# Kernel tuning notes

Measured on AMD Instinct MI355X. Metric: run time of the kernel, lower is better.

The kernel has to match this reference:

```python
import jax, jax.numpy as jnp
import numpy as np

IN_FEATURES = 4096
OUT_FEATURES = 8192
GROUP_SIZE = 16
NUM_GROUPS = IN_FEATURES * OUT_FEATURES // GROUP_SIZE  # 2_097_152


def block_dequantize_2bit(packed, normalization):
    # packed: [G, group_size//4] int32 holding uint8 values; norm: [G, 1] fp16
    shifts = jnp.arange(4, dtype=packed.dtype) * 2  # bit offsets 0,2,4,6
    # unpacked column 4k+i comes from packed column k, bits 2i..2i+1
    u = ((packed[:, :, None] >> shifts) & 3).astype(jnp.float32)  # [G, gs/4, 4]
    u = u.reshape(packed.shape[0], -1)  # [G, group_size]
    norm = normalization.astype(jnp.float32)
    return (u / 3.0) * (2.0 * norm) - norm  # [G, group_size]


def setup_inputs() -> dict:
    key = jax.random.key(0)
    k_x, k_q, k_n, k_b = jax.random.split(key, 4)
    x = jax.random.normal(k_x, (256, IN_FEATURES), dtype=jnp.float32)
    # packed 2-bit weights: random bytes (store as int32 for clean bit ops in jax)
    weight_q2 = jax.random.randint(k_q, (NUM_GROUPS, GROUP_SIZE // 4), 0, 256, dtype=jnp.int32)
    # per-group normalization (abs-max), positive, fp16 as in the module buffer
    weight_norm = (jax.random.uniform(k_n, (NUM_GROUPS, 1), dtype=jnp.float32) * 0.05 + 1e-4).astype(jnp.float16)
    bias = jax.random.normal(k_b, (OUT_FEATURES,), dtype=jnp.float32) * 0.01
    return {"x": x, "weight_q2": weight_q2, "weight_norm": weight_norm, "bias": bias}


def reference(x, weight_q2, weight_norm, bias):
    weight = block_dequantize_2bit(weight_q2, weight_norm).reshape(OUT_FEATURES, IN_FEATURES)
    return jnp.dot(x.astype(jnp.float32), weight.T) + bias
```

## Files before the change

### kernel.cpp

```cpp
#include <hip/hip_runtime.h>
#include <hip/hip_bf16.h>
#include <hip/hip_fp16.h>

#define IN_F   4096
#define OUT_F  8192
#define M_ROWS 256
#define SLAB   128
#define NSLAB  16

typedef __attribute__((ext_vector_type(8))) short  short8;
typedef __attribute__((ext_vector_type(4))) float  float4v;

union BF8 { uint4 u; short8 s; };

typedef __attribute__((address_space(1))) const unsigned int glb_uint;
typedef __attribute__((address_space(3))) unsigned int       lds_uint;

__device__ inline void gld_lds16(const void* g, void* l) {
    __builtin_amdgcn_global_load_lds((glb_uint*)g, (lds_uint*)l, 16, 0, 0);
}

__device__ inline unsigned int pack_bf16(float lo, float hi) {
    return __builtin_amdgcn_perm(__float_as_uint(hi), __float_as_uint(lo), 0x07060302u);
}

__global__ void cvt_x_kernel(const float* __restrict__ x, unsigned short* __restrict__ xb) {
    int i = blockIdx.x * blockDim.x + threadIdx.x;
    if (i < (M_ROWS * IN_F) / 4) {
        float4 v = ((const float4*)x)[i];
        uint2 o;
        o.x = pack_bf16(v.x, v.y);
        o.y = pack_bf16(v.z, v.w);
        ((uint2*)xb)[i] = o;
    }
}

template <bool XB>
__global__ __launch_bounds__(512, 4) void gemm2bit_kernel(
    const float*           __restrict__ xf,
    const unsigned short*  __restrict__ xb,
    const int*             __restrict__ wq,
    const void*            __restrict__ wnorm,
    const float*           __restrict__ bias,
    float*                 __restrict__ out)
{
    __shared__ unsigned short ldsA[2][2][64 * SLAB];

    const int t    = threadIdx.x;
    const int n0   = blockIdx.x * 64;
    const int m0   = blockIdx.y * 64;
    const int wave = t >> 6;
    const int lane = t & 63;
    const int gw   = wave & 3;
    const int grp  = wave >> 2;
    const int l15  = lane & 15;
    const int quad = lane >> 4;

    const float cand0 = *(const float*)wnorm;
    const bool  nf32  = (cand0 > 1e-5f && cand0 < 0.1f);
    const float*  nF = (const float*)wnorm;
    const __half* nH = (const __half*)wnorm;

    const int   ncol = n0 + gw * 16 + l15;
    const float bv   = bias[ncol];
    const int   kgrp = grp * (IN_F / 2);

    const int* wqW  = wq + ncol * (IN_F / 4) + (kgrp >> 2) + quad * 2;
    const int  nrmW = ncol * (IN_F / 16) + (kgrp >> 4) + (quad >> 1);

    const int srow4 = lane >> 4;
    const int sj    = lane & 15;

    int stv[4];
#pragma unroll
    for (int ks = 0; ks < 4; ++ks) {
        const int c = ks * 4 + quad;
        stv[ks] = ((c & 8) | ((c ^ (l15 & 7)) & 7)) * 8;
    }
    int fb[4];
#pragma unroll
    for (int i = 0; i < 4; ++i) fb[i] = (i * 16 + l15) * SLAB;

    float4v acc[4] = {};

    auto stage = [&](int s, int b) {
        const int kbase = kgrp + s * SLAB;
        if constexpr (XB) {
#pragma unroll
            for (int c = 0; c < 4; ++c) {
                const int R  = gw * 16 + c * 4 + srow4;
                const int lc = (sj & 8) | ((sj ^ (R & 7)) & 7);
                const unsigned short* g = xb + (m0 + R) * IN_F + kbase + lc * 8;
                gld_lds16(g, &ldsA[grp][b][(gw * 16 + c * 4) * SLAB]);
            }
        } else {
#pragma unroll
            for (int c = 0; c < 4; ++c) {
                const int R  = gw * 16 + c * 4 + srow4;
                const int lc = (sj & 8) | ((sj ^ (R & 7)) & 7);
                const float4* g = (const float4*)(xf + (m0 + R) * IN_F + kbase + lc * 8);
                float4 v0 = g[0], v1 = g[1];
                uint4 o;
                o.x = pack_bf16(v0.x, v0.y); o.y = pack_bf16(v0.z, v0.w);
                o.z = pack_bf16(v1.x, v1.y); o.w = pack_bf16(v1.z, v1.w);
                *(uint4*)&ldsA[grp][b][R * SLAB + sj * 8] = o;
            }
        }
    };

    auto load_b = [&](int s, int2 (&q)[4], float (&n)[4]) {
#pragma unroll
        for (int ks = 0; ks < 4; ++ks) {
            q[ks] = *(const int2*)(wqW + s * 32 + ks * 8);
            const int gi = nrmW + s * 8 + ks * 2;
            n[ks] = nf32 ? nF[gi] : __half2float(nH[gi]);
        }
    };

    stage(0, 0);
    int2  qn[4];
    float nn[4];
    load_b(0, qn, nn);

    for (int s = 0; s < NSLAB; ++s) {
        __syncthreads();

        if (s + 1 < NSLAB) stage(s + 1, (s + 1) & 1);

        int2  qc[4];
        float nc[4];
#pragma unroll
        for (int ks = 0; ks < 4; ++ks) { qc[ks] = qn[ks]; nc[ks] = nn[ks]; }
        const int sl = (s + 1 < NSLAB) ? (s + 1) : s;
        load_b(sl, qn, nn);

        const unsigned short* A = ldsA[grp][s & 1];
#pragma unroll
        for (int ks = 0; ks < 4; ++ks) {
            const float nnv = nc[ks];
            const float sc  = nnv * (2.0f / 3.0f);
            const int qx = qc[ks].x, qy = qc[ks].y;

            float f0 = fmaf((float)((qx      ) & 3), sc, -nnv);
            float f1 = fmaf((float)((qx >>  2) & 3), sc, -nnv);
            float f2 = fmaf((float)((qx >>  4) & 3), sc, -nnv);
            float f3 = fmaf((float)((qx >>  6) & 3), sc, -nnv);
            float f4 = fmaf((float)((qy      ) & 3), sc, -nnv);
            float f5 = fmaf((float)((qy >>  2) & 3), sc, -nnv);
            float f6 = fmaf((float)((qy >>  4) & 3), sc, -nnv);
            float f7 = fmaf((float)((qy >>  6) & 3), sc, -nnv);

            BF8 bb;
            bb.u.x = pack_bf16(f0, f1);
            bb.u.y = pack_bf16(f2, f3);
            bb.u.z = pack_bf16(f4, f5);
            bb.u.w = pack_bf16(f6, f7);

#pragma unroll
            for (int i = 0; i < 4; ++i) {
                short8 a = *(const short8*)&A[fb[i] + stv[ks]];
                acc[i] = __builtin_amdgcn_mfma_f32_16x16x32_bf16(a, bb.s, acc[i], 0, 0, 0);
            }
        }
    }

    __syncthreads();
    float* red = (float*)&ldsA[0][0][0];
    if (grp == 1) {
#pragma unroll
        for (int i = 0; i < 4; ++i)
            *(float4*)&red[(gw * 64 + lane) * 16 + i * 4] = *(float4*)&acc[i];
    }
    __syncthreads();
    if (grp == 0) {
#pragma unroll
        for (int i = 0; i < 4; ++i) {
            const float4 o = *(const float4*)&red[(gw * 64 + lane) * 16 + i * 4];
            const int row0 = m0 + i * 16 + quad * 4;
            out[(row0 + 0) * OUT_F + ncol] = acc[i][0] + o.x + bv;
            out[(row0 + 1) * OUT_F + ncol] = acc[i][1] + o.y + bv;
            out[(row0 + 2) * OUT_F + ncol] = acc[i][2] + o.z + bv;
            out[(row0 + 3) * OUT_F + ncol] = acc[i][3] + o.w + bv;
        }
    }
}

extern "C" void kernel_launch(void* const* d_in, const int* in_sizes, int n_in,
                              void* d_out, int out_size, void* d_ws, size_t ws_size,
                              hipStream_t stream) {
    const float* x    = (const float*)d_in[0];
    const int*   wq   = (const int*)d_in[1];
    const void*  wn   = (const void*)d_in[2];
    const float* bias = (const float*)d_in[3];
    float*       out  = (float*)d_out;

    const bool use_ws = ws_size >= (size_t)(M_ROWS * IN_F * sizeof(unsigned short));

    dim3 grid(OUT_F / 64, M_ROWS / 64);

    if (use_ws) {
        unsigned short* xb = (unsigned short*)d_ws;
        cvt_x_kernel<<<dim3((M_ROWS * IN_F / 4 + 255) / 256), 256, 0, stream>>>(x, xb);
        gemm2bit_kernel<true><<<grid, 512, 0, stream>>>(nullptr, xb, wq, wn, bias, out);
    } else {
        gemm2bit_kernel<false><<<grid, 512, 0, stream>>>(x, nullptr, wq, wn, bias, out);
    }
}
```

Measured before the change: 152.9 us.

## Transpose packed weights and norms per call for coalesced 32x32 MFMA GEMM

Adds per-call kernels that transpose the packed 2-bit weights and the per-group norms into K-major layouts in workspace. A new GEMM kernel then reads them coalesced across output columns. It uses 32x32x16 bf16 MFMA and splits K four ways across waves, reducing partials through LDS. The transposes add extra full passes over the weight (about 32 MB read and 32 MB written) and a fp32 norm copy on every call, in exchange for better access patterns in the main kernel.

```diff
diff --git a/kernel.cpp b/kernel.cpp
--- a/kernel.cpp
+++ b/kernel.cpp
@@ -5,11 +5,10 @@
 #define IN_F   4096
 #define OUT_F  8192
 #define M_ROWS 256
-#define SLAB   128
-#define NSLAB  16
-
-typedef __attribute__((ext_vector_type(8))) short  short8;
-typedef __attribute__((ext_vector_type(4))) float  float4v;
+
+typedef __attribute__((ext_vector_type(8)))  short short8;
+typedef __attribute__((ext_vector_type(4)))  float float4v;
+typedef __attribute__((ext_vector_type(16))) float float16v;
 
 union BF8 { uint4 u; short8 s; };
 
@@ -23,6 +22,7 @@
 __device__ inline unsigned int pack_bf16(float lo, float hi) {
     return __builtin_amdgcn_perm(__float_as_uint(hi), __float_as_uint(lo), 0x07060302u);
 }
+
 
 __global__ void cvt_x_kernel(const float* __restrict__ x, unsigned short* __restrict__ xb) {
     int i = blockIdx.x * blockDim.x + threadIdx.x;
@@ -35,6 +35,196 @@
     }
 }
 
+__global__ __launch_bounds__(256) void transpose_wq_kernel(
+    const int* __restrict__ wq, int* __restrict__ wqT) {
+    __shared__ int tile[64][65];
+    const int t   = threadIdx.x;
+    const int kq0 = blockIdx.x * 64;
+    const int n0  = blockIdx.y * 64;
+    {
+        const int r  = t >> 4;
+        const int c4 = (t & 15) * 4;
+#pragma unroll
+        for (int it = 0; it < 4; ++it) {
+            const int rr = it * 16 + r;
+            const int4 v = *(const int4*)(wq + (n0 + rr) * (IN_F / 4) + kq0 + c4);
+            tile[rr][c4 + 0] = v.x; tile[rr][c4 + 1] = v.y;
+            tile[rr][c4 + 2] = v.z; tile[rr][c4 + 3] = v.w;
+        }
+    }
+    __syncthreads();
+    {
+        const int kr = t >> 6;
+        const int nc = t & 63;
+#pragma unroll
+        for (int it = 0; it < 16; ++it) {
+            const int kk = it * 4 + kr;
+            wqT[(kq0 + kk) * OUT_F + n0 + nc] = tile[nc][kk];
+        }
+    }
+}
+
+__global__ __launch_bounds__(256) void transpose_nrm_kernel(
+    const void* __restrict__ nrm, float* __restrict__ nT) {
+    __shared__ float tile[64][65];
+    const float cand0 = *(const float*)nrm;
+    const bool  nf32  = (cand0 > 1e-5f && cand0 < 0.1f);
+    const float*  nF = (const float*)nrm;
+    const __half* nH = (const __half*)nrm;
+    const int t   = threadIdx.x;
+    const int kg0 = blockIdx.x * 64;
+    const int n0  = blockIdx.y * 64;
+#pragma unroll
+    for (int it = 0; it < 16; ++it) {
+        const int idx = it * 256 + t;
+        const int r = idx >> 6, c = idx & 63;
+        const int gi = (n0 + r) * (IN_F / 16) + kg0 + c;
+        tile[r][c] = nf32 ? nF[gi] : __half2float(nH[gi]);
+    }
+    __syncthreads();
+#pragma unroll
+    for (int it = 0; it < 16; ++it) {
+        const int idx = it * 256 + t;
+        const int kr = idx >> 6, nc = idx & 63;
+        nT[(kg0 + kr) * OUT_F + n0 + nc] = tile[nc][kr];
+    }
+}
+
+__global__ __launch_bounds__(512, 4) void gemm2bit_t_kernel(
+    const unsigned short* __restrict__ xb,
+    const int*            __restrict__ wqT,
+    const float*          __restrict__ nT,
+    const float*          __restrict__ bias,
+    float*                __restrict__ out)
+{
+    __shared__ unsigned short smA[4][2][64 * 64];
+
+    const int t    = threadIdx.x;
+    const int wave = t >> 6;
+    const int lane = t & 63;
+    const int nw   = wave & 1;
+    const int kg   = wave >> 1;
+    const int n0   = blockIdx.x * 64;
+    const int m0   = blockIdx.y * 64;
+    const int l31  = lane & 31;
+    const int kh   = lane >> 5;
+
+    const int   ncol = n0 + nw * 32 + l31;
+    const float bv   = bias[ncol];
+    const int   kbase = kg * 1024;
+
+    const int*   qptr = wqT + ((kbase >> 2) + kh * 2) * OUT_F + ncol;
+    const float* nptr = nT  + (kbase >> 4) * OUT_F + ncol;
+
+    const int srow = nw * 32 + (lane >> 3);
+    const int schk = lane & 7;
+    const unsigned short* gA =
+        xb + (m0 + srow) * IN_F + kbase + ((schk ^ (srow & 7)) << 3);
+
+    const int fswz  = l31 & 7;
+    const int frow0 = l31 * 64;
+    const int frow1 = (32 + l31) * 64;
+
+    float16v acc0 = {}, acc1 = {};
+
+    auto stage = [&](int s, int b) {
+        unsigned short* dst = &smA[kg][b][(nw * 32) * 64];
+        const unsigned short* src = gA + s * 64;
+#pragma unroll
+        for (int c = 0; c < 4; ++c)
+            gld_lds16(src + c * 8 * IN_F, dst + c * 8 * 64);
+    };
+
+    int qA[4], qB[4]; float nv[4];
+    auto load_b = [&](int s) {
+#pragma unroll
+        for (int w = 0; w < 4; ++w) {
+            const int g16 = s * 4 + w;
+            qA[w] = qptr[(g16 * 4) * OUT_F];
+            qB[w] = qptr[(g16 * 4 + 1) * OUT_F];
+            nv[w] = nptr[g16 * OUT_F];
+        }
+    };
+
+    stage(0, 0);
+    load_b(0);
+
+    for (int s = 0; s < 16; ++s) {
+        __syncthreads();
+
+        if (s + 1 < 16) stage(s + 1, (s + 1) & 1);
+
+        int qAc[4], qBc[4]; float nvc[4];
+#pragma unroll
+        for (int w = 0; w < 4; ++w) { qAc[w] = qA[w]; qBc[w] = qB[w]; nvc[w] = nv[w]; }
+        load_b((s + 1 < 16) ? s + 1 : s);
+
+        const unsigned short* A = smA[kg][s & 1];
+#pragma unroll
+        for (int w = 0; w < 4; ++w) {
+            const float nn = nvc[w];
+            const float sc = nn * (2.0f / 3.0f);
+            const int qx = qAc[w], qy = qBc[w];
+
+            float f0 = fmaf((float)((qx      ) & 3), sc, -nn);
+            float f1 = fmaf((float)((qx >>  2) & 3), sc, -nn);
+            float f2 = fmaf((float)((qx >>  4) & 3), sc, -nn);
+            float f3 = fmaf((float)((qx >>  6) & 3), sc, -nn);
+            float f4 = fmaf((float)((qy      ) & 3), sc, -nn);
+            float f5 = fmaf((float)((qy >>  2) & 3), sc, -nn);
+            float f6 = fmaf((float)((qy >>  4) & 3), sc, -nn);
+            float f7 = fmaf((float)((qy >>  6) & 3), sc, -nn);
+
+            BF8 bb;
+            bb.u.x = pack_bf16(f0, f1);
+            bb.u.y = pack_bf16(f2, f3);
+            bb.u.z = pack_bf16(f4, f5);
+            bb.u.w = pack_bf16(f6, f7);
+
+            const int co = ((w * 2 + kh) ^ fswz) << 3;
+            short8 a0 = *(const short8*)&A[frow0 + co];
+            acc0 = __builtin_amdgcn_mfma_f32_32x32x16_bf16(a0, bb.s, acc0, 0, 0, 0);
+            short8 a1 = *(const short8*)&A[frow1 + co];
+            acc1 = __builtin_amdgcn_mfma_f32_32x32x16_bf16(a1, bb.s, acc1, 0, 0, 0);
+        }
+    }
+
+    __syncthreads();
+    float4* red = (float4*)&smA[0][0][0];
+    if (kg != 0) {
+        const int base = wave * 64 + lane;
+#pragma unroll
+        for (int j4 = 0; j4 < 4; ++j4) {
+            float4 v0 = { acc0[j4*4+0], acc0[j4*4+1], acc0[j4*4+2], acc0[j4*4+3] };
+            float4 v1 = { acc1[j4*4+0], acc1[j4*4+1], acc1[j4*4+2], acc1[j4*4+3] };
+            red[(j4    ) * 512 + base] = v0;
+            red[(j4 + 4) * 512 + base] = v1;
+        }
+    }
+    __syncthreads();
+    if (kg == 0) {
+#pragma unroll
+        for (int p = 1; p < 4; ++p) {
+            const int base = (p * 2 + nw) * 64 + lane;
+#pragma unroll
+            for (int j4 = 0; j4 < 4; ++j4) {
+                const float4 v0 = red[(j4    ) * 512 + base];
+                const float4 v1 = red[(j4 + 4) * 512 + base];
+                acc0[j4*4+0] += v0.x; acc0[j4*4+1] += v0.y; acc0[j4*4+2] += v0.z; acc0[j4*4+3] += v0.w;
+                acc1[j4*4+0] += v1.x; acc1[j4*4+1] += v1.y; acc1[j4*4+2] += v1.z; acc1[j4*4+3] += v1.w;
+            }
+        }
+#pragma unroll
+        for (int r = 0; r < 16; ++r) {
+            const int row = (r & 3) + 8 * (r >> 2) + 4 * kh;
+            out[(m0 + row) * OUT_F + ncol]      = acc0[r] + bv;
+            out[(m0 + 32 + row) * OUT_F + ncol] = acc1[r] + bv;
+        }
+    }
+}
+
+#define SLAB   128
+#define NSLAB  16
 template <bool XB>
 __global__ __launch_bounds__(512, 4) void gemm2bit_kernel(
     const float*           __restrict__ xf,
@@ -45,7 +235,6 @@
     float*                 __restrict__ out)
 {
     __shared__ unsigned short ldsA[2][2][64 * SLAB];
-
     const int t    = threadIdx.x;
     const int n0   = blockIdx.x * 64;
     const int m0   = blockIdx.y * 64;
@@ -55,22 +244,17 @@
     const int grp  = wave >> 2;
     const int l15  = lane & 15;
     const int quad = lane >> 4;
-
     const float cand0 = *(const float*)wnorm;
     const bool  nf32  = (cand0 > 1e-5f && cand0 < 0.1f);
     const float*  nF = (const float*)wnorm;
     const __half* nH = (const __half*)wnorm;
-
     const int   ncol = n0 + gw * 16 + l15;
     const float bv   = bias[ncol];
     const int   kgrp = grp * (IN_F / 2);
-
     const int* wqW  = wq + ncol * (IN_F / 4) + (kgrp >> 2) + quad * 2;
     const int  nrmW = ncol * (IN_F / 16) + (kgrp >> 4) + (quad >> 1);
-
     const int srow4 = lane >> 4;
     const int sj    = lane & 15;
-
     int stv[4];
 #pragma unroll
     for (int ks = 0; ks < 4; ++ks) {
@@ -80,9 +264,7 @@
     int fb[4];
 #pragma unroll
     for (int i = 0; i < 4; ++i) fb[i] = (i * 16 + l15) * SLAB;
-
     float4v acc[4] = {};
-
     auto stage = [&](int s, int b) {
         const int kbase = kgrp + s * SLAB;
         if constexpr (XB) {
@@ -107,7 +289,6 @@
             }
         }
     };
-
     auto load_b = [&](int s, int2 (&q)[4], float (&n)[4]) {
 #pragma unroll
         for (int ks = 0; ks < 4; ++ks) {
@@ -116,31 +297,23 @@
             n[ks] = nf32 ? nF[gi] : __half2float(nH[gi]);
         }
     };
-
     stage(0, 0);
-    int2  qn[4];
-    float nn[4];
+    int2 qn[4]; float nn[4];
     load_b(0, qn, nn);
-
     for (int s = 0; s < NSLAB; ++s) {
         __syncthreads();
-
         if (s + 1 < NSLAB) stage(s + 1, (s + 1) & 1);
-
-        int2  qc[4];
-        float nc[4];
+        int2 qc[4]; float nc[4];
 #pragma unroll
         for (int ks = 0; ks < 4; ++ks) { qc[ks] = qn[ks]; nc[ks] = nn[ks]; }
         const int sl = (s + 1 < NSLAB) ? (s + 1) : s;
         load_b(sl, qn, nn);
-
         const unsigned short* A = ldsA[grp][s & 1];
 #pragma unroll
         for (int ks = 0; ks < 4; ++ks) {
             const float nnv = nc[ks];
             const float sc  = nnv * (2.0f / 3.0f);
             const int qx = qc[ks].x, qy = qc[ks].y;
-
             float f0 = fmaf((float)((qx      ) & 3), sc, -nnv);
             float f1 = fmaf((float)((qx >>  2) & 3), sc, -nnv);
             float f2 = fmaf((float)((qx >>  4) & 3), sc, -nnv);
@@ -149,13 +322,11 @@
             float f5 = fmaf((float)((qy >>  2) & 3), sc, -nnv);
             float f6 = fmaf((float)((qy >>  4) & 3), sc, -nnv);
             float f7 = fmaf((float)((qy >>  6) & 3), sc, -nnv);
-
             BF8 bb;
             bb.u.x = pack_bf16(f0, f1);
             bb.u.y = pack_bf16(f2, f3);
             bb.u.z = pack_bf16(f4, f5);
             bb.u.w = pack_bf16(f6, f7);
-
 #pragma unroll
             for (int i = 0; i < 4; ++i) {
                 short8 a = *(const short8*)&A[fb[i] + stv[ks]];
@@ -163,7 +334,6 @@
             }
         }
     }
-
     __syncthreads();
     float* red = (float*)&ldsA[0][0][0];
     if (grp == 1) {
@@ -194,15 +364,26 @@
     const float* bias = (const float*)d_in[3];
     float*       out  = (float*)d_out;
 
-    const bool use_ws = ws_size >= (size_t)(M_ROWS * IN_F * sizeof(unsigned short));
-
-    dim3 grid(OUT_F / 64, M_ROWS / 64);
-
-    if (use_ws) {
+    const size_t XB_BYTES  = (size_t)M_ROWS * IN_F * 2;
+    const size_t WQT_BYTES = (size_t)(IN_F / 4) * OUT_F * 4;
+    const size_t NT_BYTES  = (size_t)(IN_F / 16) * OUT_F * 4;
+    const size_t FULL_WS   = XB_BYTES + WQT_BYTES + NT_BYTES;
+
+    dim3 grid64(OUT_F / 64, M_ROWS / 64);
+
+    if (ws_size >= FULL_WS) {
+        unsigned short* xb  = (unsigned short*)d_ws;
+        int*            wqT = (int*)  ((char*)d_ws + XB_BYTES);
+        float*          nTp = (float*)((char*)d_ws + XB_BYTES + WQT_BYTES);
+        cvt_x_kernel<<<dim3((M_ROWS * IN_F / 4 + 255) / 256), 256, 0, stream>>>(x, xb);
+        transpose_wq_kernel<<<dim3((IN_F / 4) / 64, OUT_F / 64), 256, 0, stream>>>(wq, wqT);
+        transpose_nrm_kernel<<<dim3((IN_F / 16) / 64, OUT_F / 64), 256, 0, stream>>>(wn, nTp);
+        gemm2bit_t_kernel<<<grid64, 512, 0, stream>>>(xb, wqT, nTp, bias, out);
+    } else if (ws_size >= XB_BYTES) {
         unsigned short* xb = (unsigned short*)d_ws;
         cvt_x_kernel<<<dim3((M_ROWS * IN_F / 4 + 255) / 256), 256, 0, stream>>>(x, xb);
-        gemm2bit_kernel<true><<<grid, 512, 0, stream>>>(nullptr, xb, wq, wn, bias, out);
+        gemm2bit_kernel<true><<<grid64, 512, 0, stream>>>(nullptr, xb, wq, wn, bias, out);
     } else {
-        gemm2bit_kernel<false><<<grid, 512, 0, stream>>>(x, nullptr, wq, wn, bias, out);
-    }
-}
+        gemm2bit_kernel<false><<<grid64, 512, 0, stream>>>(x, nullptr, wq, wn, bias, out);
+    }
+}
```

Result: faster. 130.1 us (-14.9%).
